# Optimization experiments

Measured on AMD Instinct MI355X. Metric: run time of the kernel, lower is better.

The kernel has to match this reference:

```python
import jax, jax.numpy as jnp
import numpy as np

B, N, K = 8, 1024, 20


def _w(key, o, i):
    return jax.random.normal(key, (o, i), dtype=jnp.float32) * (1.0 / np.sqrt(i))


def setup_inputs() -> dict:
    key = jax.random.key(0)
    ks = iter(jax.random.split(key, 64))
    d = {"inputs": jax.random.normal(next(ks), (B, 3, N, 1), dtype=jnp.float32)}
    shapes = {
        "he_w1": (32, 12), "he_w2": (64, 32), "hn_w1": (32, 67), "hn_w2": (64, 32),
        "b1e_w1": (48, 192), "b1e_w2": (128, 48), "b1n_w1": (48, 192), "b1n_w2": (128, 48),
        "b2e_w1": (96, 384), "b2e_w2": (192, 96), "b2n_w1": (96, 320), "b2n_w2": (192, 96),
        "f_w": (512, 384), "p1_w": (256, 512), "p2_w": (128, 256), "p3_w": (40, 128),
    }
    for name, (o, i) in shapes.items():
        d[name] = _w(next(ks), o, i)
        d[name.replace("_w", "_b")] = jnp.zeros((o,), dtype=jnp.float32)
    return d


def _conv(x, w, b):
    # BasicConv with norm=None: 1x1 Conv2d + bias. x: [B,C,N,k]
    return jnp.einsum('bcnk,oc->bonk', x, w) + b[None, :, None, None]


def _conv_relu(x, w, b):
    return jax.nn.relu(_conv(x, w, b))


def _gather(x, idx):
    # batched_index_select: x [B,C,N,1], idx [B,N,k] -> [B,C,N,k]
    b, c, n, _ = x.shape
    k = idx.shape[-1]
    out = jnp.take_along_axis(x[:, :, :, 0], idx.reshape(b, 1, n * k), axis=2)
    return out.reshape(b, c, n, k)


def _knn(x, k):
    # DenseKnnGraph: x [B,C,N,1] -> (nn_idx, center_idx), each [B,N,k]
    xt = jnp.transpose(x[:, :, :, 0], (0, 2, 1))  # [B,N,C]
    sq = jnp.sum(xt * xt, axis=-1, keepdims=True)
    dist = sq - 2.0 * jnp.einsum('bnc,bmc->bnm', xt, xt) + jnp.transpose(sq, (0, 2, 1))
    _, nn_idx = jax.lax.top_k(-dist, k)
    center = jnp.broadcast_to(jnp.arange(x.shape[2])[None, :, None], nn_idx.shape)
    return nn_idx, center


def _mp(nf, e_ij, nn_idx, center, ew1, eb1, ew2, eb2, nw1, nb1, nw2, nb2):
    # MessagePassing block (Kearnes et al. style)
    h_i = _gather(nf, center)  # [B,Cin,N,k]
    h_j = _gather(nf, nn_idx)
    e_p = _conv_relu(_conv_relu(jnp.concatenate([e_ij, h_i, h_j], axis=1), ew1, eb1), ew2, eb2)
    m = jnp.broadcast_to(jnp.sum(e_p, axis=3, keepdims=True),
                         e_p.shape[:3] + (h_i.shape[-1],))
    h_p = _conv_relu(_conv_relu(jnp.concatenate([h_i, m], axis=1), nw1, nb1), nw2, nb2)
    return h_p[:, :, :, 0:1], e_p


def reference(inputs, he_w1, he_b1, he_w2, he_b2, hn_w1, hn_b1, hn_w2, hn_b2,
              b1e_w1, b1e_b1, b1e_w2, b1e_b2, b1n_w1, b1n_b1, b1n_w2, b1n_b2,
              b2e_w1, b2e_b1, b2e_w2, b2e_b2, b2n_w1, b2n_b1, b2n_w2, b2n_b2,
              f_w, f_b, p1_w, p1_b, p2_w, p2_b, p3_w, p3_b):
    nn_idx, center = _knn(inputs[:, 0:3], K)
    # initial edge features: (h_i, h_i - h_j) on xyz-KNN graph
    gh_i = _gather(inputs, center)
    gh_j = _gather(inputs, nn_idx)
    e_ij = jnp.concatenate([gh_i, gh_i - gh_j], axis=1)  # [B, 2*in, N, k]
    h1, e1 = _mp(inputs, e_ij, nn_idx, center, he_w1, he_b1, he_w2, he_b2, hn_w1, hn_b1, hn_w2, hn_b2)
    h2, e2 = _mp(h1, e1, nn_idx, center, b1e_w1, b1e_b1, b1e_w2, b1e_b2, b1n_w1, b1n_b1, b1n_w2, b1n_b2)
    h3, e3 = _mp(h2, e2, nn_idx, center, b2e_w1, b2e_b1, b2e_w2, b2e_b2, b2n_w1, b2n_b1, b2n_w2, b2n_b2)
    feats = jnp.concatenate([h1, h2, h3], axis=1)  # [B, 384, N, 1]
    fus = _conv_relu(feats, f_w, f_b)  # [B, 512, N, 1]
    pooled = jnp.max(fus, axis=(2, 3), keepdims=True)  # max_pool2d over [N,1]
    # prediction head (dropout = identity at inference)
    pred = _conv(_conv_relu(_conv_relu(pooled, p1_w, p1_b), p2_w, p2_b), p3_w, p3_b)
    return pred[:, :, :, 0], inputs  # (logits [B,n_classes,1], edge_features)
```

## Files before the change

kernel.cpp:

```cpp
#include <hip/hip_runtime.h>

#define BDIM 8
#define NDIM 1024
#define KNN 20

typedef unsigned short u16;
typedef float f32x4 __attribute__((ext_vector_type(4)));
typedef short short8 __attribute__((ext_vector_type(8)));
typedef unsigned short ushort8 __attribute__((ext_vector_type(8)));

__device__ inline u16 f2bf(float f) {
  unsigned u = __float_as_uint(f);
  unsigned r = (u + 0x7fffu + ((u >> 16) & 1u)) >> 16;
  return (u16)r;
}
__device__ inline float bf2f(u16 v) {
  return __uint_as_float(((unsigned)v) << 16);
}

__global__ __launch_bounds__(256) void knn_wcvt(
    const float* __restrict__ x, int* __restrict__ nn,
    const float* __restrict__ w1_3, const float* __restrict__ w2_3,
    const float* __restrict__ w1_2, const float* __restrict__ w2_2,
    const float* __restrict__ hn_w1, const float* __restrict__ f_w,
    const float* __restrict__ he_w1, const float* __restrict__ he_w2,
    const float* __restrict__ bn_w1, const float* __restrict__ bn_w2,
    u16* __restrict__ w1b3e, u16* __restrict__ wpq3, u16* __restrict__ w2b3,
    u16* __restrict__ w1b2e, u16* __restrict__ wpq2, u16* __restrict__ w2b2,
    float* __restrict__ w1p1, u16* __restrict__ fwb,
    u16* __restrict__ w1b1, u16* __restrict__ w2b1,
    u16* __restrict__ wn1b, u16* __restrict__ wn2b, int* __restrict__ pooled) {
  const int tid = threadIdx.x;
  if (blockIdx.x >= BDIM * 256) {
    const int idx = (blockIdx.x - BDIM * 256) * 256 + tid;
    if (idx < 512 * 384) fwb[idx] = f2bf(f_w[idx]);
    if (idx < 96 * 128) {
      int oc = idx >> 7, c = idx & 127;
      w1b3e[idx] = f2bf(w1_3[oc * 384 + c]);
    }
    if (idx < 192 * 128) {
      int n = idx >> 7, c = idx & 127;
      wpq3[idx] = f2bf(n < 96 ? w1_3[n * 384 + 128 + c]
                              : w1_3[(n - 96) * 384 + 256 + c]);
    }
    if (idx < 192 * 96) w2b3[idx] = f2bf(w2_3[idx]);
    if (idx < 48 * 64) {
      int oc = idx >> 6, c = idx & 63;
      w1b2e[idx] = f2bf(w1_2[oc * 192 + c]);
    }
    if (idx < 96 * 64) {
      int n = idx >> 6, c = idx & 63;
      wpq2[idx] = f2bf(n < 48 ? w1_2[n * 192 + 64 + c]
                              : w1_2[(n - 48) * 192 + 128 + c]);
    }
    if (idx < 128 * 64) {
      int oc = idx >> 6, i = idx & 63;
      w2b2[idx] = (i < 48) ? f2bf(w2_2[oc * 48 + i]) : (u16)0;
    }
    if (idx < 32 * 68) {
      int oc = idx / 68, c = idx - oc * 68;
      w1p1[idx] = (c < 67) ? hn_w1[oc * 67 + c] : 0.0f;
    }
    if (idx < 32 * 32) {
      int oc = idx >> 5, c = idx & 31;
      w1b1[idx] = (c < 12) ? f2bf(he_w1[oc * 12 + c]) : (u16)0;
    }
    if (idx < 64 * 32) w2b1[idx] = f2bf(he_w2[idx]);
    if (idx < 96 * 320) wn1b[idx] = f2bf(bn_w1[idx]);
    if (idx < 192 * 96) wn2b[idx] = f2bf(bn_w2[idx]);
    if (idx < BDIM * 512) pooled[idx] = 0;
    return;
  }
  {
#pragma clang fp contract(off)
    __shared__ float xs0[NDIM], xs1[NDIM], xs2[NDIM], sq[NDIM];
    const int lane = tid & 63;
    const int w = tid >> 6;
    const int b = blockIdx.x >> 8;
    const int n = ((blockIdx.x & 255) << 2) + w;
    for (int i = tid; i < NDIM; i += 256) {
      float a0 = x[(b * 3 + 0) * NDIM + i];
      float a1 = x[(b * 3 + 1) * NDIM + i];
      float a2 = x[(b * 3 + 2) * NDIM + i];
      xs0[i] = a0; xs1[i] = a1; xs2[i] = a2;
      sq[i] = (a0 * a0 + a1 * a1) + a2 * a2;
    }
    __syncthreads();
    const float xn0 = xs0[n], xn1 = xs1[n], xn2 = xs2[n], sqn = sq[n];
    float dl[16];
#pragma unroll
    for (int t = 0; t < 16; ++t) {
      int m = t * 64 + lane;
      float dot = (xn0 * xs0[m] + xn1 * xs1[m]) + xn2 * xs2[m];
      dl[t] = (sqn - 2.0f * dot) + sq[m];
    }
    int* nnrow = &nn[(b * NDIM + n) * KNN];
    for (int r = 0; r < KNN; ++r) {
      float bd = dl[0];
      int bt = 0;
#pragma unroll
      for (int t = 1; t < 16; ++t) {
        if (dl[t] < bd) { bd = dl[t]; bt = t; }
      }
      int bi = bt * 64 + lane;
#pragma unroll
      for (int off = 1; off < 64; off <<= 1) {
        float pd = __shfl_xor(bd, off);
        int pi = __shfl_xor(bi, off);
        if (pd < bd || (pd == bd && pi < bi)) { bd = pd; bi = pi; }
      }
      if (lane == 0) nnrow[r] = bi;
      if ((bi & 63) == lane) {
        int wt = bi >> 6;
#pragma unroll
        for (int t = 0; t < 16; ++t) {
          if (t == wt) dl[t] = 3.4e38f;
        }
      }
    }
  }
}

template <int PTS, int CE, int CMID, int COUT, bool WRITE_E, bool FIRST, bool FUSE_N>
__global__ __launch_bounds__(256) void edge_mfma(
    const u16* __restrict__ eprev, const float* __restrict__ finput,
    const int* __restrict__ nnb, const u16* __restrict__ w1b,
    const float* __restrict__ b1v, const u16* __restrict__ w2b,
    const float* __restrict__ b2v, const u16* __restrict__ pq,
    u16* __restrict__ eout, float* __restrict__ mout,
    const float* __restrict__ hprev, const u16* __restrict__ wn1b,
    const float* __restrict__ bn1v, const u16* __restrict__ wn2b,
    const float* __restrict__ bn2v, float* __restrict__ h3out) {
  constexpr int K2 = (CMID + 31) & ~31;
  constexpr int NPQ = 2 * CMID;
  constexpr int MT = PTS * KNN;
  constexpr int MTL = MT / 16;
  constexpr int XPB = CE + 8;
  constexpr int QYP = K2 + 8;
  __shared__ __align__(16) char smem[MT * XPB * 2 + MT * QYP * 2];
  u16* Xs = (u16*)smem;
  u16* QY = (u16*)(smem + (size_t)MT * XPB * 2);
  float* msum = (float*)smem;
  u16* Xn = (u16*)(smem + 3072);
  u16* Y1n = (u16*)(smem + 3072 + 16 * 328 * 2);
  __shared__ float pld[FIRST ? 8 : PTS * CMID];
  const int tid = threadIdx.x;
  const int lane = tid & 63;
  const int wv = tid >> 6;
  const int q = lane >> 4;
  const int bn0 = blockIdx.x * PTS;
  const int b = bn0 >> 10;
  if constexpr (FIRST) {
    for (int idx = tid; idx < MT * (CE / 8); idx += 256) {
      int p = idx / (CE / 8), kc = idx - p * (CE / 8);
      int k0 = kc * 8;
      int bn = bn0 + p / KNN;
      int n = bn & (NDIM - 1);
      int j = nnb[(size_t)bn0 * KNN + p];
      ushort8 r;
#pragma unroll
      for (int t = 0; t < 8; ++t) {
        int c = k0 + t;
        float v = 0.0f;
        if (c < 3) v = finput[(b * 3 + c) * NDIM + n];
        else if (c < 6)
          v = finput[(b * 3 + c - 3) * NDIM + n] -
              finput[(b * 3 + c - 3) * NDIM + j];
        else if (c < 9) v = finput[(b * 3 + c - 6) * NDIM + n];
        else if (c < 12) v = finput[(b * 3 + c - 9) * NDIM + j];
        r[t] = f2bf(v);
      }
      *(ushort8*)&Xs[p * XPB + k0] = r;
    }
  } else {
    constexpr int KC = CE / 8;
    for (int ch = tid; ch < MT * KC; ch += 256) {
      int p = ch / KC, kc = ch - p * KC;
      int k0 = kc * 8;
      *(uint4*)&Xs[p * XPB + k0] =
          *(const uint4*)&eprev[((size_t)blockIdx.x * MT + p) * CE + k0];
    }
    constexpr int QC = CMID / 8;
    for (int i = tid; i < MT * QC; i += 256) {
      int p = i / QC, c8 = (i - p * QC) * 8;
      int j = nnb[(size_t)bn0 * KNN + p];
      *(uint4*)&QY[p * QYP + c8] =
          *(const uint4*)&pq[((size_t)(b << 10) + j) * NPQ + CMID + c8];
    }
    if constexpr (K2 != CMID) {
      constexpr int PC = (K2 - CMID) / 8;
      for (int i = tid; i < MT * PC; i += 256) {
        int p = i / PC, c8 = CMID + (i - p * PC) * 8;
        uint4 z = {0, 0, 0, 0};
        *(uint4*)&QY[p * QYP + c8] = z;
      }
    }
    for (int i = tid; i < PTS * CMID; i += 256) {
      int pt = i / CMID, c = i - pt * CMID;
      pld[i] = bf2f(pq[(size_t)(bn0 + pt) * NPQ + c]) + b1v[c];
    }
  }
  __syncthreads();
  {
    constexpr int NT1 = CMID / 16;
    constexpr int J1 = MTL * NT1;
    constexpr int KS1 = CE / 32;
    for (int job = wv; job < J1; job += 4) {
      int mt = job / NT1, nt = job - mt * NT1;
      int row = mt * 16 + (lane & 15);
      int ncol = nt * 16 + (lane & 15);
      int kb = q * 8;
      f32x4 acc = {0.f, 0.f, 0.f, 0.f};
      const u16* ap = &Xs[row * XPB + kb];
      const u16* bp = &w1b[(size_t)ncol * CE + kb];
#pragma unroll
      for (int ks = 0; ks < KS1; ++ks) {
        short8 a = *(const short8*)(ap + ks * 32);
        short8 bb = *(const short8*)(bp + ks * 32);
        acc = __builtin_amdgcn_mfma_f32_16x16x32_bf16(a, bb, acc, 0, 0, 0);
      }
      int m0 = mt * 16 + q * 4;
      if constexpr (FIRST) {
        float bias = b1v[ncol];
#pragma unroll
        for (int r = 0; r < 4; ++r) {
          float yv = fmaxf(acc[r] + bias, 0.0f);
          QY[(m0 + r) * QYP + ncol] = f2bf(yv);
        }
      } else {
        int pt = m0 / KNN;
        float padd = pld[pt * CMID + ncol];
#pragma unroll
        for (int r = 0; r < 4; ++r) {
          int m = m0 + r;
          float qadd = bf2f(QY[m * QYP + ncol]);
          float yv = fmaxf(acc[r] + padd + qadd, 0.0f);
          QY[m * QYP + ncol] = f2bf(yv);
        }
      }
    }
  }
  __syncthreads();
  {
    constexpr int NT2 = COUT / 16;
    constexpr int KS2 = K2 / 32;
    for (int nt = wv; nt < NT2; nt += 4) {
      int ncol = nt * 16 + (lane & 15);
      int kb = q * 8;
      short8 bfrag[KS2];
      const u16* bp = &w2b[(size_t)ncol * K2 + kb];
#pragma unroll
      for (int ks = 0; ks < KS2; ++ks)
        bfrag[ks] = *(const short8*)(bp + ks * 32);
      float bias = b2v[ncol];
      float s[PTS];
#pragma unroll
      for (int pt = 0; pt < PTS; ++pt) s[pt] = 0.0f;
#pragma unroll
      for (int mt = 0; mt < MTL; ++mt) {
        f32x4 acc = {0.f, 0.f, 0.f, 0.f};
        const u16* ap = &QY[(mt * 16 + (lane & 15)) * QYP + kb];
#pragma unroll
        for (int ks = 0; ks < KS2; ++ks) {
          short8 a = *(const short8*)(ap + ks * 32);
          acc = __builtin_amdgcn_mfma_f32_16x16x32_bf16(a, bfrag[ks], acc, 0, 0, 0);
        }
        int m0 = mt * 16 + q * 4;
        float part = 0.0f;
#pragma unroll
        for (int r = 0; r < 4; ++r) {
          float yv = fmaxf(acc[r] + bias, 0.0f);
          if (WRITE_E)
            eout[((size_t)blockIdx.x * MT + m0 + r) * COUT + ncol] = f2bf(yv);
          part += yv;
        }
        int ptA = (4 * mt) / 5;
        int ptB = (4 * mt + 3) / 5;
        int qb = 5 * ptB - 4 * mt;
#pragma unroll
        for (int pt2 = 0; pt2 < PTS; ++pt2) {
          if (pt2 == ptA && ptA == ptB) s[pt2] += part;
          else if (pt2 == ptA) s[pt2] += (q < qb) ? part : 0.0f;
          else if (pt2 == ptB) s[pt2] += (q < qb) ? 0.0f : part;
        }
      }
#pragma unroll
      for (int pt = 0; pt < PTS; ++pt) {
        float sv = s[pt];
        sv += __shfl_xor(sv, 16);
        sv += __shfl_xor(sv, 32);
        if (lane < 16) {
          if constexpr (FUSE_N)
            msum[pt * COUT + nt * 16 + lane] = sv;
          else
            mout[(size_t)(bn0 + pt) * COUT + nt * 16 + lane] = sv;
        }
      }
    }
  }
  if constexpr (FUSE_N) {
    constexpr int XNP = 328;
    constexpr int Y1NP = 104;
    __syncthreads();
    for (int i = tid; i < 4 * 41; i += 256) {
      int p = i / 41, kc = i - p * 41;
      int k0 = kc * 8;
      ushort8 r;
      if (kc < 16) {
        const float* src = &hprev[(size_t)(bn0 + p) * 128 + k0];
        float4 f0 = *(const float4*)src;
        float4 f1 = *(const float4*)(src + 4);
        r[0] = f2bf(f0.x); r[1] = f2bf(f0.y); r[2] = f2bf(f0.z); r[3] = f2bf(f0.w);
        r[4] = f2bf(f1.x); r[5] = f2bf(f1.y); r[6] = f2bf(f1.z); r[7] = f2bf(f1.w);
      } else if (kc < 40) {
        const float* src = &msum[p * 192 + (k0 - 128)];
#pragma unroll
        for (int t = 0; t < 8; ++t) r[t] = f2bf(src[t]);
      } else {
#pragma unroll
        for (int t = 0; t < 8; ++t) r[t] = 0;
      }
      *(ushort8*)&Xn[p * XNP + k0] = r;
    }
    __syncthreads();
    for (int nt = wv; nt < 6; nt += 4) {
      int ncol = nt * 16 + (lane & 15);
      int kb = q * 8;
      f32x4 acc = {0.f, 0.f, 0.f, 0.f};
      const u16* ap = &Xn[(lane & 15) * XNP + kb];
      const u16* bp = &wn1b[(size_t)ncol * 320 + kb];
#pragma unroll
      for (int ks = 0; ks < 10; ++ks) {
        short8 a = *(const short8*)(ap + ks * 32);
        short8 bb = *(const short8*)(bp + ks * 32);
        acc = __builtin_amdgcn_mfma_f32_16x16x32_bf16(a, bb, acc, 0, 0, 0);
      }
      float bias = bn1v[ncol];
      int m0 = q * 4;
#pragma unroll
      for (int r = 0; r < 4; ++r)
        Y1n[(m0 + r) * Y1NP + ncol] = f2bf(fmaxf(acc[r] + bias, 0.0f));
    }
    __syncthreads();
    for (int nt = wv; nt < 12; nt += 4) {
      int ncol = nt * 16 + (lane & 15);
      int kb = q * 8;
      f32x4 acc = {0.f, 0.f, 0.f, 0.f};
      const u16* ap = &Y1n[(lane & 15) * Y1NP + kb];
      const u16* bp = &wn2b[(size_t)ncol * 96 + kb];
#pragma unroll
      for (int ks = 0; ks < 3; ++ks) {
        short8 a = *(const short8*)(ap + ks * 32);
        short8 bb = *(const short8*)(bp + ks * 32);
        acc = __builtin_amdgcn_mfma_f32_16x16x32_bf16(a, bb, acc, 0, 0, 0);
      }
      float bias = bn2v[ncol];
      int m0 = q * 4;
#pragma unroll
      for (int r = 0; r < 4; ++r) {
        int m = m0 + r;
        if (m < 4)
          h3out[(size_t)(bn0 + m) * 192 + ncol] = fmaxf(acc[r] + bias, 0.0f);
      }
    }
  }
}

template <int TP, int CH, int CM, int CINP, int CMID, int COUT, int NPQ, bool FIRSTH>
__global__ __launch_bounds__(256) void node_conv(
    const float* __restrict__ h, const float* __restrict__ inputs,
    const float* __restrict__ mbuf, const float* __restrict__ w1p,
    const float* __restrict__ b1v, const float* __restrict__ w2,
    const float* __restrict__ b2v, float* __restrict__ hout,
    const u16* __restrict__ wpq, u16* __restrict__ pq) {
  constexpr int CIN = CH + CM;
  constexpr int XP = CINP + 4;
  constexpr int Y1P = CMID + 4;
  constexpr int PG = TP / 4;
  constexpr int HP = COUT + 8;
  __shared__ float Xs[TP * XP];
  __shared__ float Y1s[TP * Y1P];
  __shared__ u16 Hb[(NPQ > 0) ? TP * HP : 8];
  const int tid = threadIdx.x;
  const int bn0 = blockIdx.x * TP;
  if constexpr (FIRSTH) {
    for (int idx = tid; idx < TP * CIN; idx += 256) {
      int p = idx / CIN, c = idx - p * CIN;
      int bn = bn0 + p;
      int b = bn >> 10, n = bn & (NDIM - 1);
      Xs[p * XP + c] = (c < CH) ? inputs[(b * 3 + c) * NDIM + n]
                                : mbuf[(size_t)bn * CM + (c - CH)];
    }
    if constexpr (CINP > CIN) {
      constexpr int PAD = CINP - CIN;
      for (int idx = tid; idx < TP * PAD; idx += 256) {
        int p = idx / PAD, c = CIN + idx % PAD;
        Xs[p * XP + c] = 0.0f;
      }
    }
  } else {
    constexpr int C4 = CIN / 4;
    for (int idx = tid; idx < TP * C4; idx += 256) {
      int p = idx / C4, c = (idx - p * C4) * 4;
      int bn = bn0 + p;
      float4 v = (c < CH) ? *(const float4*)&h[(size_t)bn * CH + c]
                          : *(const float4*)&mbuf[(size_t)bn * CM + (c - CH)];
      *(float4*)&Xs[p * XP + c] = v;
    }
  }
  __syncthreads();
  {
    constexpr int NT1 = PG * (CMID / 4);
    for (int t = tid; t < NT1; t += 256) {
      int pg = t % PG, og = t / PG;
      float acc[4][4];
#pragma unroll
      for (int j = 0; j < 4; ++j) {
        float bj = b1v[og * 4 + j];
#pragma unroll
        for (int i = 0; i < 4; ++i) acc[i][j] = bj;
      }
      for (int cin = 0; cin < CINP; cin += 4) {
        float4 xr[4], wr[4];
#pragma unroll
        for (int i = 0; i < 4; ++i)
          xr[i] = *(const float4*)&Xs[(pg * 4 + i) * XP + cin];
#pragma unroll
        for (int j = 0; j < 4; ++j)
          wr[j] = *(const float4*)&w1p[(size_t)(og * 4 + j) * CINP + cin];
#pragma unroll
        for (int i = 0; i < 4; ++i)
#pragma unroll
          for (int j = 0; j < 4; ++j) {
            acc[i][j] += xr[i].x * wr[j].x;
            acc[i][j] += xr[i].y * wr[j].y;
            acc[i][j] += xr[i].z * wr[j].z;
            acc[i][j] += xr[i].w * wr[j].w;
          }
      }
#pragma unroll
      for (int i = 0; i < 4; ++i)
#pragma unroll
        for (int j = 0; j < 4; ++j)
          Y1s[(pg * 4 + i) * Y1P + og * 4 + j] = fmaxf(acc[i][j], 0.0f);
    }
  }
  __syncthreads();
  {
    constexpr int NT2 = PG * (COUT / 4);
    for (int t = tid; t < NT2; t += 256) {
      int pg = t % PG, og = t / PG;
      float acc[4][4];
#pragma unroll
      for (int j = 0; j < 4; ++j) {
        float bj = b2v[og * 4 + j];
#pragma unroll
        for (int i = 0; i < 4; ++i) acc[i][j] = bj;
      }
      for (int cin = 0; cin < CMID; cin += 4) {
        float4 xr[4], wr[4];
#pragma unroll
        for (int i = 0; i < 4; ++i)
          xr[i] = *(const float4*)&Y1s[(pg * 4 + i) * Y1P + cin];
#pragma unroll
        for (int j = 0; j < 4; ++j)
          wr[j] = *(const float4*)&w2[(size_t)(og * 4 + j) * CMID + cin];
#pragma unroll
        for (int i = 0; i < 4; ++i)
#pragma unroll
          for (int j = 0; j < 4; ++j) {
            acc[i][j] += xr[i].x * wr[j].x;
            acc[i][j] += xr[i].y * wr[j].y;
            acc[i][j] += xr[i].z * wr[j].z;
            acc[i][j] += xr[i].w * wr[j].w;
          }
      }
#pragma unroll
      for (int i = 0; i < 4; ++i) {
        int bn = bn0 + pg * 4 + i;
#pragma unroll
        for (int j = 0; j < 4; ++j) {
          float v = fmaxf(acc[i][j], 0.0f);
          hout[(size_t)bn * COUT + og * 4 + j] = v;
          if constexpr (NPQ > 0) Hb[(pg * 4 + i) * HP + og * 4 + j] = f2bf(v);
        }
      }
    }
  }
  if constexpr (NPQ > 0) {
    __syncthreads();
    const int lane = tid & 63;
    const int wv = tid >> 6;
    constexpr int NT = NPQ / 16;
    constexpr int JOBS = (TP / 16) * NT;
    constexpr int KS = COUT / 32;
    for (int job = wv; job < JOBS; job += 4) {
      int mt = job / NT, nt = job - mt * NT;
      int row = mt * 16 + (lane & 15);
      int ncol = nt * 16 + (lane & 15);
      int kb = (lane >> 4) * 8;
      f32x4 acc = {0.f, 0.f, 0.f, 0.f};
      const u16* ap = &Hb[row * HP + kb];
      const u16* bp = &wpq[(size_t)ncol * COUT + kb];
#pragma unroll
      for (int ks = 0; ks < KS; ++ks) {
        short8 a = *(const short8*)(ap + ks * 32);
        short8 bb = *(const short8*)(bp + ks * 32);
        acc = __builtin_amdgcn_mfma_f32_16x16x32_bf16(a, bb, acc, 0, 0, 0);
      }
      int m0 = mt * 16 + (lane >> 4) * 4;
#pragma unroll
      for (int r = 0; r < 4; ++r)
        pq[(size_t)(bn0 + m0 + r) * NPQ + ncol] = f2bf(acc[r]);
    }
  }
}

__global__ __launch_bounds__(256) void fuse_pool_mfma(
    const float* __restrict__ h1, const float* __restrict__ h2,
    const float* __restrict__ h3, const u16* __restrict__ fwb,
    const float* __restrict__ fb, int* __restrict__ pooled) {
  constexpr int CIN = 384, COUT = 512, TP = 32;
  constexpr int XPB = CIN + 8;
  __shared__ u16 Xs[TP * XPB];
  __shared__ int pmax[COUT];
  const int tid = threadIdx.x;
  const int lane = tid & 63;
  const int wv = tid >> 6;
  const int bn0 = blockIdx.x * TP;
  const int b = bn0 >> 10;
  for (int i = tid; i < COUT; i += 256) pmax[i] = 0;
  constexpr int KC = CIN / 8;
  for (int ch = tid; ch < TP * KC; ch += 256) {
    int p = ch / KC, kc = ch - p * KC;
    int k0 = kc * 8;
    int bn = bn0 + p;
    const float* src;
    if (k0 < 64) src = &h1[(size_t)bn * 64 + k0];
    else if (k0 < 192) src = &h2[(size_t)bn * 128 + (k0 - 64)];
    else src = &h3[(size_t)bn * 192 + (k0 - 192)];
    float4 f0 = *(const float4*)src;
    float4 f1 = *(const float4*)(src + 4);
    ushort8 r;
    r[0] = f2bf(f0.x); r[1] = f2bf(f0.y); r[2] = f2bf(f0.z); r[3] = f2bf(f0.w);
    r[4] = f2bf(f1.x); r[5] = f2bf(f1.y); r[6] = f2bf(f1.z); r[7] = f2bf(f1.w);
    *(ushort8*)&Xs[p * XPB + k0] = r;
  }
  __syncthreads();
  constexpr int NT = COUT / 16;
  constexpr int JOBS = (TP / 16) * NT;
  constexpr int KS = CIN / 32;
  for (int job = wv; job < JOBS; job += 4) {
    int mt = job / NT, nt = job - mt * NT;
    int row = mt * 16 + (lane & 15);
    int ncol = nt * 16 + (lane & 15);
    int kb = (lane >> 4) * 8;
    f32x4 acc = {0.f, 0.f, 0.f, 0.f};
    const u16* ap = &Xs[row * XPB + kb];
    const u16* bp = &fwb[(size_t)ncol * CIN + kb];
#pragma unroll
    for (int ks = 0; ks < KS; ++ks) {
      short8 a = *(const short8*)(ap + ks * 32);
      short8 bb = *(const short8*)(bp + ks * 32);
      acc = __builtin_amdgcn_mfma_f32_16x16x32_bf16(a, bb, acc, 0, 0, 0);
    }
    float bias = fb[ncol];
    float v = fmaxf(fmaxf(acc[0], acc[1]), fmaxf(acc[2], acc[3]));
    v = fmaxf(v + bias, 0.0f);
    v = fmaxf(v, __shfl_xor(v, 16));
    v = fmaxf(v, __shfl_xor(v, 32));
    if (lane < 16) atomicMax(&pmax[ncol], __float_as_int(v));
  }
  __syncthreads();
  for (int i = tid; i < COUT; i += 256)
    atomicMax(&pooled[b * COUT + i], pmax[i]);
}

__global__ __launch_bounds__(256) void head_kernel(
    const int* __restrict__ pooledi, const float* __restrict__ p1w,
    const float* __restrict__ p1b, const float* __restrict__ p2w,
    const float* __restrict__ p2b, const float* __restrict__ p3w,
    const float* __restrict__ p3b, const float* __restrict__ inputs,
    float* __restrict__ out) {
  const int tid = threadIdx.x;
  if (blockIdx.x >= BDIM) {
    int idx = (blockIdx.x - BDIM) * 256 + tid;
    if (idx < (BDIM * 3 * NDIM) / 4) {
      const float4* src = (const float4*)inputs;
      float4* dst = (float4*)(out + BDIM * 40);
      dst[idx] = src[idx];
    }
    return;
  }
  __shared__ float xs[512], y1[256], y2[128];
  const int b = blockIdx.x;
  for (int i = tid; i < 512; i += 256) xs[i] = __int_as_float(pooledi[b * 512 + i]);
  __syncthreads();
  {
    float acc = p1b[tid];
    for (int c = 0; c < 512; ++c) acc += xs[c] * p1w[tid * 512 + c];
    y1[tid] = fmaxf(acc, 0.0f);
  }
  __syncthreads();
  if (tid < 128) {
    float acc = p2b[tid];
    for (int c = 0; c < 256; ++c) acc += y1[c] * p2w[tid * 256 + c];
    y2[tid] = fmaxf(acc, 0.0f);
  }
  __syncthreads();
  if (tid < 40) {
    float acc = p3b[tid];
    for (int c = 0; c < 128; ++c) acc += y2[c] * p3w[tid * 128 + c];
    out[b * 40 + tid] = acc;
  }
}

extern "C" void kernel_launch(void* const* d_in, const int* in_sizes, int n_in,
                              void* d_out, int out_size, void* d_ws,
                              size_t ws_size, hipStream_t stream) {
  const float* inputs = (const float*)d_in[0];
  const float* he_w1 = (const float*)d_in[1];
  const float* he_b1 = (const float*)d_in[2];
  const float* he_w2 = (const float*)d_in[3];
  const float* he_b2 = (const float*)d_in[4];
  const float* hn_w1 = (const float*)d_in[5];
  const float* hn_b1 = (const float*)d_in[6];
  const float* hn_w2 = (const float*)d_in[7];
  const float* hn_b2 = (const float*)d_in[8];
  const float* b1e_w1 = (const float*)d_in[9];
  const float* b1e_b1 = (const float*)d_in[10];
  const float* b1e_w2 = (const float*)d_in[11];
  const float* b1e_b2 = (const float*)d_in[12];
  const float* b1n_w1 = (const float*)d_in[13];
  const float* b1n_b1 = (const float*)d_in[14];
  const float* b1n_w2 = (const float*)d_in[15];
  const float* b1n_b2 = (const float*)d_in[16];
  const float* b2e_w1 = (const float*)d_in[17];
  const float* b2e_b1 = (const float*)d_in[18];
  const float* b2e_w2 = (const float*)d_in[19];
  const float* b2e_b2 = (const float*)d_in[20];
  const float* b2n_w1 = (const float*)d_in[21];
  const float* b2n_b1 = (const float*)d_in[22];
  const float* b2n_w2 = (const float*)d_in[23];
  const float* b2n_b2 = (const float*)d_in[24];
  const float* f_w = (const float*)d_in[25];
  const float* f_b = (const float*)d_in[26];
  const float* p1_w = (const float*)d_in[27];
  const float* p1_b = (const float*)d_in[28];
  const float* p2_w = (const float*)d_in[29];
  const float* p2_b = (const float*)d_in[30];
  const float* p3_w = (const float*)d_in[31];
  const float* p3_b = (const float*)d_in[32];
  float* out = (float*)d_out;

  char* ws = (char*)d_ws;
  size_t off = 0;
  auto alloc = [&](size_t bytes) {
    void* p = ws + off;
    off += (bytes + 255) & ~(size_t)255;
    return p;
  };
  int* nn = (int*)alloc((size_t)BDIM * NDIM * KNN * 4);
  float* m1 = (float*)alloc((size_t)BDIM * NDIM * 64 * 4);
  float* h1 = (float*)alloc((size_t)BDIM * NDIM * 64 * 4);
  u16* e1 = (u16*)alloc((size_t)BDIM * NDIM * KNN * 64 * 2);
  float* m2 = (float*)alloc((size_t)BDIM * NDIM * 128 * 4);
  float* h2 = (float*)alloc((size_t)BDIM * NDIM * 128 * 4);
  u16* e2 = (u16*)alloc((size_t)BDIM * NDIM * KNN * 128 * 2);
  float* h3 = (float*)alloc((size_t)BDIM * NDIM * 192 * 4);
  u16* pq2 = (u16*)alloc((size_t)BDIM * NDIM * 96 * 2);
  u16* pq3 = (u16*)alloc((size_t)BDIM * NDIM * 192 * 2);
  int* pooled = (int*)alloc((size_t)BDIM * 512 * 4);
  u16* w1b3e = (u16*)alloc((size_t)96 * 128 * 2);
  u16* wpq3 = (u16*)alloc((size_t)192 * 128 * 2);
  u16* w2b3 = (u16*)alloc((size_t)192 * 96 * 2);
  u16* w1b2e = (u16*)alloc((size_t)48 * 64 * 2);
  u16* wpq2 = (u16*)alloc((size_t)96 * 64 * 2);
  u16* w2b2 = (u16*)alloc((size_t)128 * 64 * 2);
  float* w1p1 = (float*)alloc((size_t)32 * 68 * 4);
  u16* fwb = (u16*)alloc((size_t)512 * 384 * 2);
  u16* w1b1 = (u16*)alloc((size_t)32 * 32 * 2);
  u16* w2b1 = (u16*)alloc((size_t)64 * 32 * 2);
  u16* wn1b = (u16*)alloc((size_t)96 * 320 * 2);
  u16* wn2b = (u16*)alloc((size_t)192 * 96 * 2);

  knn_wcvt<<<BDIM * 256 + 768, 256, 0, stream>>>(
      inputs, nn, b2e_w1, b2e_w2, b1e_w1, b1e_w2, hn_w1, f_w, he_w1, he_w2,
      b2n_w1, b2n_w2, w1b3e, wpq3, w2b3, w1b2e, wpq2, w2b2, w1p1, fwb, w1b1,
      w2b1, wn1b, wn2b, pooled);

  edge_mfma<4, 32, 32, 64, true, true, false><<<BDIM * NDIM / 4, 256, 0, stream>>>(
      nullptr, inputs, nn, w1b1, he_b1, w2b1, he_b2, nullptr, e1, m1, nullptr,
      nullptr, nullptr, nullptr, nullptr, nullptr);
  node_conv<64, 3, 64, 68, 32, 64, 96, true><<<BDIM * NDIM / 64, 256, 0, stream>>>(
      nullptr, inputs, m1, w1p1, hn_b1, hn_w2, hn_b2, h1, wpq2, pq2);

  edge_mfma<4, 64, 48, 128, true, false, false><<<BDIM * NDIM / 4, 256, 0, stream>>>(
      e1, nullptr, nn, w1b2e, b1e_b1, w2b2, b1e_b2, pq2, e2, m2, nullptr,
      nullptr, nullptr, nullptr, nullptr, nullptr);
  node_conv<32, 64, 128, 192, 48, 128, 192, false><<<BDIM * NDIM / 32, 256, 0, stream>>>(
      h1, nullptr, m2, b1n_w1, b1n_b1, b1n_w2, b1n_b2, h2, wpq3, pq3);

  edge_mfma<4, 128, 96, 192, false, false, true><<<BDIM * NDIM / 4, 256, 0, stream>>>(
      e2, nullptr, nn, w1b3e, b2e_b1, w2b3, b2e_b2, pq3, nullptr, nullptr, h2,
      wn1b, b2n_b1, wn2b, b2n_b2, h3);

  fuse_pool_mfma<<<BDIM * NDIM / 32, 256, 0, stream>>>(h1, h2, h3, fwb, f_b,
                                                       pooled);
  head_kernel<<<BDIM + 24, 256, 0, stream>>>(pooled, p1_w, p1_b, p2_w, p2_b,
                                             p3_w, p3_b, inputs, out);
}
```

Measured before the change: 238.2 us.

## Move block-3 node MLP from edge kernel into fuse-pool kernel

The final node convolution (two MFMA GEMMs over h2 and the aggregated messages) moves out of the third edge kernel and into the fuse/pool kernel. There it runs on 32-point tiles and writes its output directly into the shared-memory input of the fusion GEMM. Before, that node MLP ran on 16-row MFMA tiles holding only 4 valid points, so most of that work was wasted. The change also drops the h3 round trip through global memory. In exchange, the edge kernel now writes an fp32 message buffer m3 that the fusion kernel reads back, and the fusion kernel does more serial work per block.

```diff
diff --git a/kernel.cpp b/kernel.cpp
--- a/kernel.cpp
+++ b/kernel.cpp
@@ -121,28 +121,21 @@
   }
 }
 
-template <int PTS, int CE, int CMID, int COUT, bool WRITE_E, bool FIRST, bool FUSE_N>
+template <int PTS, int CE, int CMID, int COUT, bool WRITE_E, bool FIRST>
 __global__ __launch_bounds__(256) void edge_mfma(
     const u16* __restrict__ eprev, const float* __restrict__ finput,
     const int* __restrict__ nnb, const u16* __restrict__ w1b,
     const float* __restrict__ b1v, const u16* __restrict__ w2b,
     const float* __restrict__ b2v, const u16* __restrict__ pq,
-    u16* __restrict__ eout, float* __restrict__ mout,
-    const float* __restrict__ hprev, const u16* __restrict__ wn1b,
-    const float* __restrict__ bn1v, const u16* __restrict__ wn2b,
-    const float* __restrict__ bn2v, float* __restrict__ h3out) {
+    u16* __restrict__ eout, float* __restrict__ mout) {
   constexpr int K2 = (CMID + 31) & ~31;
   constexpr int NPQ = 2 * CMID;
   constexpr int MT = PTS * KNN;
   constexpr int MTL = MT / 16;
   constexpr int XPB = CE + 8;
   constexpr int QYP = K2 + 8;
-  __shared__ __align__(16) char smem[MT * XPB * 2 + MT * QYP * 2];
-  u16* Xs = (u16*)smem;
-  u16* QY = (u16*)(smem + (size_t)MT * XPB * 2);
-  float* msum = (float*)smem;
-  u16* Xn = (u16*)(smem + 3072);
-  u16* Y1n = (u16*)(smem + 3072 + 16 * 328 * 2);
+  __shared__ u16 Xs[MT * XPB];
+  __shared__ u16 QY[MT * QYP];
   __shared__ float pld[FIRST ? 8 : PTS * CMID];
   const int tid = threadIdx.x;
   const int lane = tid & 63;
@@ -289,78 +282,8 @@
         float sv = s[pt];
         sv += __shfl_xor(sv, 16);
         sv += __shfl_xor(sv, 32);
-        if (lane < 16) {
-          if constexpr (FUSE_N)
-            msum[pt * COUT + nt * 16 + lane] = sv;
-          else
-            mout[(size_t)(bn0 + pt) * COUT + nt * 16 + lane] = sv;
-        }
-      }
-    }
-  }
-  if constexpr (FUSE_N) {
-    constexpr int XNP = 328;
-    constexpr int Y1NP = 104;
-    __syncthreads();
-    for (int i = tid; i < 4 * 41; i += 256) {
-      int p = i / 41, kc = i - p * 41;
-      int k0 = kc * 8;
-      ushort8 r;
-      if (kc < 16) {
-        const float* src = &hprev[(size_t)(bn0 + p) * 128 + k0];
-        float4 f0 = *(const float4*)src;
-        float4 f1 = *(const float4*)(src + 4);
-        r[0] = f2bf(f0.x); r[1] = f2bf(f0.y); r[2] = f2bf(f0.z); r[3] = f2bf(f0.w);
-        r[4] = f2bf(f1.x); r[5] = f2bf(f1.y); r[6] = f2bf(f1.z); r[7] = f2bf(f1.w);
-      } else if (kc < 40) {
-        const float* src = &msum[p * 192 + (k0 - 128)];
-#pragma unroll
-        for (int t = 0; t < 8; ++t) r[t] = f2bf(src[t]);
-      } else {
-#pragma unroll
-        for (int t = 0; t < 8; ++t) r[t] = 0;
-      }
-      *(ushort8*)&Xn[p * XNP + k0] = r;
-    }
-    __syncthreads();
-    for (int nt = wv; nt < 6; nt += 4) {
-      int ncol = nt * 16 + (lane & 15);
-      int kb = q * 8;
-      f32x4 acc = {0.f, 0.f, 0.f, 0.f};
-      const u16* ap = &Xn[(lane & 15) * XNP + kb];
-      const u16* bp = &wn1b[(size_t)ncol * 320 + kb];
-#pragma unroll
-      for (int ks = 0; ks < 10; ++ks) {
-        short8 a = *(const short8*)(ap + ks * 32);
-        short8 bb = *(const short8*)(bp + ks * 32);
-        acc = __builtin_amdgcn_mfma_f32_16x16x32_bf16(a, bb, acc, 0, 0, 0);
-      }
-      float bias = bn1v[ncol];
-      int m0 = q * 4;
-#pragma unroll
-      for (int r = 0; r < 4; ++r)
-        Y1n[(m0 + r) * Y1NP + ncol] = f2bf(fmaxf(acc[r] + bias, 0.0f));
-    }
-    __syncthreads();
-    for (int nt = wv; nt < 12; nt += 4) {
-      int ncol = nt * 16 + (lane & 15);
-      int kb = q * 8;
-      f32x4 acc = {0.f, 0.f, 0.f, 0.f};
-      const u16* ap = &Y1n[(lane & 15) * Y1NP + kb];
-      const u16* bp = &wn2b[(size_t)ncol * 96 + kb];
-#pragma unroll
-      for (int ks = 0; ks < 3; ++ks) {
-        short8 a = *(const short8*)(ap + ks * 32);
-        short8 bb = *(const short8*)(bp + ks * 32);
-        acc = __builtin_amdgcn_mfma_f32_16x16x32_bf16(a, bb, acc, 0, 0, 0);
-      }
-      float bias = bn2v[ncol];
-      int m0 = q * 4;
-#pragma unroll
-      for (int r = 0; r < 4; ++r) {
-        int m = m0 + r;
-        if (m < 4)
-          h3out[(size_t)(bn0 + m) * 192 + ncol] = fmaxf(acc[r] + bias, 0.0f);
+        if (lane < 16)
+          mout[(size_t)(bn0 + pt) * COUT + nt * 16 + lane] = sv;
       }
     }
   }
@@ -518,27 +441,75 @@
 
 __global__ __launch_bounds__(256) void fuse_pool_mfma(
     const float* __restrict__ h1, const float* __restrict__ h2,
-    const float* __restrict__ h3, const u16* __restrict__ fwb,
+    const float* __restrict__ m3, const u16* __restrict__ wn1b,
+    const float* __restrict__ bn1v, const u16* __restrict__ wn2b,
+    const float* __restrict__ bn2v, const u16* __restrict__ fwb,
     const float* __restrict__ fb, int* __restrict__ pooled) {
-  constexpr int CIN = 384, COUT = 512, TP = 32;
-  constexpr int XPB = CIN + 8;
-  __shared__ u16 Xs[TP * XPB];
-  __shared__ int pmax[COUT];
+  constexpr int TP = 32;
+  constexpr int XNP = 328;
+  constexpr int Y1NP = 104;
+  constexpr int XPB = 392;
+  __shared__ __align__(16) char smem[TP * XPB * 2];
+  u16* Xs = (u16*)smem;
+  u16* Xn = (u16*)smem;
+  __shared__ u16 Y1n[TP * Y1NP];
+  __shared__ int pmax[512];
   const int tid = threadIdx.x;
   const int lane = tid & 63;
   const int wv = tid >> 6;
+  const int q = lane >> 4;
   const int bn0 = blockIdx.x * TP;
   const int b = bn0 >> 10;
-  for (int i = tid; i < COUT; i += 256) pmax[i] = 0;
-  constexpr int KC = CIN / 8;
-  for (int ch = tid; ch < TP * KC; ch += 256) {
-    int p = ch / KC, kc = ch - p * KC;
+  for (int i = tid; i < 512; i += 256) pmax[i] = 0;
+  for (int i = tid; i < TP * 41; i += 256) {
+    int p = i / 41, kc = i - p * 41;
     int k0 = kc * 8;
-    int bn = bn0 + p;
-    const float* src;
-    if (k0 < 64) src = &h1[(size_t)bn * 64 + k0];
-    else if (k0 < 192) src = &h2[(size_t)bn * 128 + (k0 - 64)];
-    else src = &h3[(size_t)bn * 192 + (k0 - 192)];
+    ushort8 r;
+    if (kc < 16) {
+      const float* src = &h2[(size_t)(bn0 + p) * 128 + k0];
+      float4 f0 = *(const float4*)src;
+      float4 f1 = *(const float4*)(src + 4);
+      r[0] = f2bf(f0.x); r[1] = f2bf(f0.y); r[2] = f2bf(f0.z); r[3] = f2bf(f0.w);
+      r[4] = f2bf(f1.x); r[5] = f2bf(f1.y); r[6] = f2bf(f1.z); r[7] = f2bf(f1.w);
+    } else if (kc < 40) {
+      const float* src = &m3[(size_t)(bn0 + p) * 192 + (k0 - 128)];
+      float4 f0 = *(const float4*)src;
+      float4 f1 = *(const float4*)(src + 4);
+      r[0] = f2bf(f0.x); r[1] = f2bf(f0.y); r[2] = f2bf(f0.z); r[3] = f2bf(f0.w);
+      r[4] = f2bf(f1.x); r[5] = f2bf(f1.y); r[6] = f2bf(f1.z); r[7] = f2bf(f1.w);
+    } else {
+#pragma unroll
+      for (int t = 0; t < 8; ++t) r[t] = 0;
+    }
+    *(ushort8*)&Xn[p * XNP + k0] = r;
+  }
+  __syncthreads();
+  for (int job = wv; job < 12; job += 4) {
+    int mt = job / 6, nt = job - mt * 6;
+    int row = mt * 16 + (lane & 15);
+    int ncol = nt * 16 + (lane & 15);
+    int kb = q * 8;
+    f32x4 acc = {0.f, 0.f, 0.f, 0.f};
+    const u16* ap = &Xn[row * XNP + kb];
+    const u16* bp = &wn1b[(size_t)ncol * 320 + kb];
+#pragma unroll
+    for (int ks = 0; ks < 10; ++ks) {
+      short8 a = *(const short8*)(ap + ks * 32);
+      short8 bb = *(const short8*)(bp + ks * 32);
+      acc = __builtin_amdgcn_mfma_f32_16x16x32_bf16(a, bb, acc, 0, 0, 0);
+    }
+    float bias = bn1v[ncol];
+    int m0 = mt * 16 + q * 4;
+#pragma unroll
+    for (int r = 0; r < 4; ++r)
+      Y1n[(m0 + r) * Y1NP + ncol] = f2bf(fmaxf(acc[r] + bias, 0.0f));
+  }
+  __syncthreads();
+  for (int i = tid; i < TP * 24; i += 256) {
+    int p = i / 24, kc = i - p * 24;
+    int k0 = kc * 8;
+    const float* src = (k0 < 64) ? &h1[(size_t)(bn0 + p) * 64 + k0]
+                                 : &h2[(size_t)(bn0 + p) * 128 + (k0 - 64)];
     float4 f0 = *(const float4*)src;
     float4 f1 = *(const float4*)(src + 4);
     ushort8 r;
@@ -546,20 +517,41 @@
     r[4] = f2bf(f1.x); r[5] = f2bf(f1.y); r[6] = f2bf(f1.z); r[7] = f2bf(f1.w);
     *(ushort8*)&Xs[p * XPB + k0] = r;
   }
-  __syncthreads();
-  constexpr int NT = COUT / 16;
-  constexpr int JOBS = (TP / 16) * NT;
-  constexpr int KS = CIN / 32;
-  for (int job = wv; job < JOBS; job += 4) {
-    int mt = job / NT, nt = job - mt * NT;
+  if (tid < TP) {
+    ushort8 z = {0, 0, 0, 0, 0, 0, 0, 0};
+    *(ushort8*)&Xs[tid * XPB + 384] = z;
+  }
+  for (int job = wv; job < 24; job += 4) {
+    int mt = job / 12, nt = job - mt * 12;
     int row = mt * 16 + (lane & 15);
     int ncol = nt * 16 + (lane & 15);
-    int kb = (lane >> 4) * 8;
+    int kb = q * 8;
+    f32x4 acc = {0.f, 0.f, 0.f, 0.f};
+    const u16* ap = &Y1n[row * Y1NP + kb];
+    const u16* bp = &wn2b[(size_t)ncol * 96 + kb];
+#pragma unroll
+    for (int ks = 0; ks < 3; ++ks) {
+      short8 a = *(const short8*)(ap + ks * 32);
+      short8 bb = *(const short8*)(bp + ks * 32);
+      acc = __builtin_amdgcn_mfma_f32_16x16x32_bf16(a, bb, acc, 0, 0, 0);
+    }
+    float bias = bn2v[ncol];
+    int m0 = mt * 16 + q * 4;
+#pragma unroll
+    for (int r = 0; r < 4; ++r)
+      Xs[(m0 + r) * XPB + 192 + ncol] = f2bf(fmaxf(acc[r] + bias, 0.0f));
+  }
+  __syncthreads();
+  for (int job = wv; job < 64; job += 4) {
+    int mt = job / 32, nt = job - mt * 32;
+    int row = mt * 16 + (lane & 15);
+    int ncol = nt * 16 + (lane & 15);
+    int kb = q * 8;
     f32x4 acc = {0.f, 0.f, 0.f, 0.f};
     const u16* ap = &Xs[row * XPB + kb];
-    const u16* bp = &fwb[(size_t)ncol * CIN + kb];
-#pragma unroll
-    for (int ks = 0; ks < KS; ++ks) {
+    const u16* bp = &fwb[(size_t)ncol * 384 + kb];
+#pragma unroll
+    for (int ks = 0; ks < 12; ++ks) {
       short8 a = *(const short8*)(ap + ks * 32);
       short8 bb = *(const short8*)(bp + ks * 32);
       acc = __builtin_amdgcn_mfma_f32_16x16x32_bf16(a, bb, acc, 0, 0, 0);
@@ -572,8 +564,8 @@
     if (lane < 16) atomicMax(&pmax[ncol], __float_as_int(v));
   }
   __syncthreads();
-  for (int i = tid; i < COUT; i += 256)
-    atomicMax(&pooled[b * COUT + i], pmax[i]);
+  for (int i = tid; i < 512; i += 256)
+    atomicMax(&pooled[b * 512 + i], pmax[i]);
 }
 
 __global__ __launch_bounds__(256) void head_kernel(
@@ -667,7 +659,7 @@
   float* m2 = (float*)alloc((size_t)BDIM * NDIM * 128 * 4);
   float* h2 = (float*)alloc((size_t)BDIM * NDIM * 128 * 4);
   u16* e2 = (u16*)alloc((size_t)BDIM * NDIM * KNN * 128 * 2);
-  float* h3 = (float*)alloc((size_t)BDIM * NDIM * 192 * 4);
+  float* m3 = (float*)alloc((size_t)BDIM * NDIM * 192 * 4);
   u16* pq2 = (u16*)alloc((size_t)BDIM * NDIM * 96 * 2);
   u16* pq3 = (u16*)alloc((size_t)BDIM * NDIM * 192 * 2);
   int* pooled = (int*)alloc((size_t)BDIM * 512 * 4);
@@ -689,24 +681,21 @@
       b2n_w1, b2n_w2, w1b3e, wpq3, w2b3, w1b2e, wpq2, w2b2, w1p1, fwb, w1b1,
       w2b1, wn1b, wn2b, pooled);
 
-  edge_mfma<4, 32, 32, 64, true, true, false><<<BDIM * NDIM / 4, 256, 0, stream>>>(
-      nullptr, inputs, nn, w1b1, he_b1, w2b1, he_b2, nullptr, e1, m1, nullptr,
-      nullptr, nullptr, nullptr, nullptr, nullptr);
+  edge_mfma<4, 32, 32, 64, true, true><<<BDIM * NDIM / 4, 256, 0, stream>>>(
+      nullptr, inputs, nn, w1b1, he_b1, w2b1, he_b2, nullptr, e1, m1);
   node_conv<64, 3, 64, 68, 32, 64, 96, true><<<BDIM * NDIM / 64, 256, 0, stream>>>(
       nullptr, inputs, m1, w1p1, hn_b1, hn_w2, hn_b2, h1, wpq2, pq2);
 
-  edge_mfma<4, 64, 48, 128, true, false, false><<<BDIM * NDIM / 4, 256, 0, stream>>>(
-      e1, nullptr, nn, w1b2e, b1e_b1, w2b2, b1e_b2, pq2, e2, m2, nullptr,
-      nullptr, nullptr, nullptr, nullptr, nullptr);
+  edge_mfma<4, 64, 48, 128, true, false><<<BDIM * NDIM / 4, 256, 0, stream>>>(
+      e1, nullptr, nn, w1b2e, b1e_b1, w2b2, b1e_b2, pq2, e2, m2);
   node_conv<32, 64, 128, 192, 48, 128, 192, false><<<BDIM * NDIM / 32, 256, 0, stream>>>(
       h1, nullptr, m2, b1n_w1, b1n_b1, b1n_w2, b1n_b2, h2, wpq3, pq3);
 
-  edge_mfma<4, 128, 96, 192, false, false, true><<<BDIM * NDIM / 4, 256, 0, stream>>>(
-      e2, nullptr, nn, w1b3e, b2e_b1, w2b3, b2e_b2, pq3, nullptr, nullptr, h2,
-      wn1b, b2n_b1, wn2b, b2n_b2, h3);
-
-  fuse_pool_mfma<<<BDIM * NDIM / 32, 256, 0, stream>>>(h1, h2, h3, fwb, f_b,
-                                                       pooled);
+  edge_mfma<4, 128, 96, 192, false, false><<<BDIM * NDIM / 4, 256, 0, stream>>>(
+      e2, nullptr, nn, w1b3e, b2e_b1, w2b3, b2e_b2, pq3, nullptr, m3);
+
+  fuse_pool_mfma<<<BDIM * NDIM / 32, 256, 0, stream>>>(
+      h1, h2, m3, wn1b, b2n_b1, wn2b, b2n_b2, fwb, f_b, pooled);
   head_kernel<<<BDIM + 24, 256, 0, stream>>>(pooled, p1_w, p1_b, p2_w, p2_b,
                                              p3_w, p3_b, inputs, out);
 }
```

Result: faster. 225.2 us (-5.5%).
